# Kernel tuning notes

Measured on AMD Instinct MI355X. Metric: run time of the kernel, lower is better.

The kernel has to match this reference:

```python
import jax, jax.numpy as jnp
import numpy as np

N_EMBD = 1024
HEAD_SIZE = 64
N_HEADS = 16
BLOCK_SIZE = 2048


def setup_inputs() -> dict:
    key = jax.random.key(0)
    ks = jax.random.split(key, 7)
    s = 0.02
    return {
        "X": jax.random.normal(ks[0], (2, BLOCK_SIZE, N_EMBD), dtype=jnp.float32),
        # per-head projection weights, torch Linear layout [out, in] stacked over heads
        "Wq": jax.random.normal(ks[1], (N_HEADS, HEAD_SIZE, N_EMBD), dtype=jnp.float32) * s,
        "Wk": jax.random.normal(ks[2], (N_HEADS, HEAD_SIZE, N_EMBD), dtype=jnp.float32) * s,
        "Wv": jax.random.normal(ks[3], (N_HEADS, HEAD_SIZE, N_EMBD), dtype=jnp.float32) * s,
        "Wp": jax.random.normal(ks[4], (N_EMBD, N_EMBD), dtype=jnp.float32) * s,
        "bp": jax.random.normal(ks[5], (N_EMBD,), dtype=jnp.float32) * s,
    }


def reference(X, Wq, Wk, Wv, Wp, bp):
    B, T, C = X.shape
    # per-head projections: [B,H,T,D]
    q = jnp.einsum("btc,hdc->bhtd", X, Wq)
    k = jnp.einsum("btc,hdc->bhtd", X, Wk)
    v = jnp.einsum("btc,hdc->bhtd", X, Wv)
    # NOTE: original scales by C**-0.5 where C = n_embd (not head_size)
    scores = jnp.einsum("bhtd,bhsd->bhts", q, k) * (C ** -0.5)  # [B,H,T,T]
    causal = jnp.tril(jnp.ones((T, T), dtype=bool))
    scores = jnp.where(causal, scores, -jnp.inf)
    weights = jax.nn.softmax(scores, axis=-1)
    out = jnp.einsum("bhts,bhsd->bhtd", weights, v)  # [B,H,T,D]
    # concat heads along last dim: [B,T,H*D]
    out = out.transpose(0, 2, 1, 3).reshape(B, T, -1)
    # output projection (dropout is identity in eval)
    return out @ Wp.T + bp
```

## Files before the change

### kernel.cpp

```cpp
#include <hip/hip_runtime.h>
#include <hip/hip_bf16.h>

typedef __bf16 bf16_t;
typedef __bf16 bf16x8 __attribute__((ext_vector_type(8)));
typedef __bf16 bf16x4 __attribute__((ext_vector_type(4)));
typedef float  f32x4  __attribute__((ext_vector_type(4)));

#define MFMA16(a,b,c) __builtin_amdgcn_mfma_f32_16x16x32_bf16(a,b,c,0,0,0)

constexpr int B_ = 2, T_ = 2048, H_ = 16, D_ = 64, C_ = 1024;
constexpr int GK = C_;

typedef const __attribute__((address_space(1))) unsigned char ga_t;
typedef __attribute__((address_space(3))) unsigned char la_t;
__device__ __forceinline__ void gld16(const void* g, void* l) {
  __builtin_amdgcn_global_load_lds((ga_t*)g, (la_t*)l, 16, 0, 0);
}

__global__ __launch_bounds__(256) void cast_all(
    const float* __restrict__ X,  const float* __restrict__ Wq,
    const float* __restrict__ Wk, const float* __restrict__ Wv,
    const float* __restrict__ Wp,
    bf16_t* __restrict__ Xb,  bf16_t* __restrict__ Wqb, bf16_t* __restrict__ Wkb,
    bf16_t* __restrict__ Wvb, bf16_t* __restrict__ Wpb)
{
  int i = blockIdx.x * 256 + threadIdx.x;
  const float* src; bf16_t* dst; int off;
  if      (i < 1048576) { src = X;  dst = Xb;  off = i; }
  else if (i < 1310720) { src = Wq; dst = Wqb; off = i - 1048576; }
  else if (i < 1572864) { src = Wk; dst = Wkb; off = i - 1310720; }
  else if (i < 1835008) { src = Wv; dst = Wvb; off = i - 1572864; }
  else                  { src = Wp; dst = Wpb; off = i - 1835008; }
  float4 v = *reinterpret_cast<const float4*>(src + (size_t)off * 4);
  bf16x4 o;
  o[0] = (bf16_t)v.x; o[1] = (bf16_t)v.y; o[2] = (bf16_t)v.z; o[3] = (bf16_t)v.w;
  *reinterpret_cast<bf16x4*>(dst + (size_t)off * 4) = o;
}

__device__ __forceinline__ void gemm_bk64_core(
    const bf16_t* __restrict__ A, const bf16_t* __restrict__ Bw,
    bf16_t* sA, bf16_t* sB, f32x4 (&acc)[4][2], int bm, int bn)
{
  const int tid  = threadIdx.x;
  const int lane = tid & 63, wid = tid >> 6;
  const int wm = wid >> 2, wn = wid & 3;
  const int g = lane >> 4, c = lane & 15;
  const int srow = tid >> 3, scc = tid & 7;
  const int rk = c & 7;

  #define STG(buf, k0)                                                        \
    { char* da = (char*)sA + (buf) * 16384;                                   \
      char* db = (char*)sB + (buf) * 16384;                                   \
      _Pragma("unroll")                                                       \
      for (int it = 0; it < 2; ++it) {                                        \
        int row = it * 64 + srow;                                             \
        int sg  = scc ^ (row & 7);                   \
        int idx = it * 512 + tid;                                             \
        gld16(A  + (size_t)(bm * 128 + row) * GK + (k0) + sg * 8, da + idx * 16); \
        gld16(Bw + (size_t)(bn * 128 + row) * GK + (k0) + sg * 8, db + idx * 16); \
      } }

  STG(0, 0);
  for (int step = 0; step < 16; ++step) {
    const int cur = step & 1;
    __syncthreads();
    if (step < 15) STG(cur ^ 1, (step + 1) * 64);

    const char* ca = (char*)sA + cur * 16384;
    const char* cb = (char*)sB + cur * 16384;
    bf16x8 af[4][2], bf[2][2];
    #pragma unroll
    for (int m = 0; m < 4; ++m) {
      int r = wm * 64 + m * 16 + c;
      #pragma unroll
      for (int ks = 0; ks < 2; ++ks)
        af[m][ks] = *reinterpret_cast<const bf16x8*>(
            ca + r * 128 + (((ks * 4 + g) ^ rk) * 16));
    }
    #pragma unroll
    for (int n = 0; n < 2; ++n) {
      int r = wn * 32 + n * 16 + c;
      #pragma unroll
      for (int ks = 0; ks < 2; ++ks)
        bf[n][ks] = *reinterpret_cast<const bf16x8*>(
            cb + r * 128 + (((ks * 4 + g) ^ rk) * 16));
    }
    __builtin_amdgcn_s_setprio(1);
    #pragma unroll
    for (int ks = 0; ks < 2; ++ks)
      #pragma unroll
      for (int m = 0; m < 4; ++m)
        #pragma unroll
        for (int n = 0; n < 2; ++n)
          acc[m][n] = MFMA16(af[m][ks], bf[n][ks], acc[m][n]);
    __builtin_amdgcn_s_setprio(0);
  }
  #undef STG
}

__global__ __launch_bounds__(512, 4) void gemm_qkv(
    const bf16_t* __restrict__ Xb,
    const bf16_t* __restrict__ Wqb, const bf16_t* __restrict__ Wkb,
    const bf16_t* __restrict__ Wvb,
    bf16_t* __restrict__ qo, bf16_t* __restrict__ ko, bf16_t* __restrict__ vto)
{
  __shared__ bf16_t sA[2][128 * 64];
  __shared__ bf16_t sB[2][128 * 64];
  f32x4 acc[4][2] = {};
  const int mode = blockIdx.z;
  const bf16_t* W = (mode == 0) ? Wqb : (mode == 1) ? Wkb : Wvb;
  gemm_bk64_core(Xb, W, &sA[0][0], &sB[0][0], acc, blockIdx.x, blockIdx.y);

  const int tid = threadIdx.x;
  const int lane = tid & 63, wid = tid >> 6;
  const int wm = wid >> 2, wn = wid & 3;
  const int g = lane >> 4, c = lane & 15;
  const float scale = (mode == 0) ? 0.04508422002778f : 1.0f;
  #pragma unroll
  for (int m = 0; m < 4; ++m) {
    #pragma unroll
    for (int n = 0; n < 2; ++n) {
      #pragma unroll
      for (int r = 0; r < 4; ++r) {
        int row = blockIdx.x * 128 + wm * 64 + m * 16 + g * 4 + r;
        int col = blockIdx.y * 128 + wn * 32 + n * 16 + c;
        int b = row >> 11, t = row & 2047;
        int h = col >> 6,  d = col & 63;
        bf16_t val = (bf16_t)(acc[m][n][r] * scale);
        if (mode == 2)
          vto[((size_t)(b * H_ + h) * D_ + d) * T_ + t] = val;
        else if (mode == 1)
          ko[((size_t)(b * H_ + h) * T_ + t) * D_ + d] = val;
        else
          qo[((size_t)(b * H_ + h) * T_ + t) * D_ + d] = val;
      }
    }
  }
}

__global__ __launch_bounds__(256, 4) void attn_fwd(
    const bf16_t* __restrict__ q, const bf16_t* __restrict__ k,
    const bf16_t* __restrict__ vt, bf16_t* __restrict__ att)
{
  __shared__ bf16_t sK[2][64 * 64], sV[2][64 * 64];
  __shared__ bf16_t sP[4][16 * 64];
  const int tid = threadIdx.x, lane = tid & 63, w = tid >> 6;
  const int g = lane >> 4, c = lane & 15;
  const int bid = blockIdx.x;
  const int qt = 31 - (bid >> 5);
  const int bh = bid & 31;
  const bf16_t* qb = q  + (size_t)bh * T_ * D_;
  const bf16_t* kb = k  + (size_t)bh * T_ * D_;
  const bf16_t* vb = vt + (size_t)bh * D_ * T_;

  bf16x8 qa[2];
  #pragma unroll
  for (int ks = 0; ks < 2; ++ks)
    qa[ks] = *reinterpret_cast<const bf16x8*>(
        qb + (size_t)(qt * 64 + w * 16 + c) * D_ + ks * 32 + g * 8);

  const int srow = tid >> 3, sgr0 = tid & 7;
  #define STAGE(buf, kt)                                                        \
    {                                                                           \
      char* kdst = (char*)sK + (size_t)(buf) * 8192;                            \
      char* vdst = (char*)sV + (size_t)(buf) * 8192;                            \
      _Pragma("unroll")                                                         \
      for (int it = 0; it < 2; ++it) {                                          \
        int idx = it * 256 + tid;                                               \
        int row = it * 32 + srow;                                               \
        int sg  = sgr0 ^ (row & 7);                                             \
        gld16(kb + (size_t)((kt) * 64 + row) * D_ + sg * 8, kdst + idx * 16);   \
        gld16(vb + (size_t)row * T_ + (kt) * 64 + sg * 8,   vdst + idx * 16);   \
      }                                                                         \
    }

  STAGE(0, 0);

  float m_r = -3.0e38f, l_r = 0.f;
  f32x4 acc_t[4] = {};
  const int rowK = c & 7;

  for (int kt = 0; kt <= qt; ++kt) {
    const int cur = kt & 1;
    __syncthreads();
    if (kt < qt) STAGE(cur ^ 1, kt + 1);

    const char* kc = (char*)sK + (size_t)cur * 8192;
    const char* vc = (char*)sV + (size_t)cur * 8192;
    bf16x8 kf[2][4], vf[2][4];
    #pragma unroll
    for (int ks = 0; ks < 2; ++ks)
      #pragma unroll
      for (int f = 0; f < 4; ++f) {
        int rb = (f * 16 + c) * 128;
        int gsw = ((ks * 4 + g) ^ rowK) * 16;
        kf[ks][f] = *reinterpret_cast<const bf16x8*>(kc + rb + gsw);
        vf[ks][f] = *reinterpret_cast<const bf16x8*>(vc + rb + gsw);
      }

    f32x4 s[4] = {};
    #pragma unroll
    for (int fj = 0; fj < 4; ++fj)
      #pragma unroll
      for (int ks = 0; ks < 2; ++ks)
        s[fj] = MFMA16(kf[ks][fj], qa[ks], s[fj]);

    if (kt == qt) {
      #pragma unroll
      for (int fj = 0; fj < 4; ++fj)
        #pragma unroll
        for (int r = 0; r < 4; ++r)
          if (fj * 16 + g * 4 + r > w * 16 + c) s[fj][r] = -1e30f;
    }

    float m01 = fmaxf(fmaxf(s[0][0], s[0][1]), fmaxf(s[0][2], s[0][3]));
    float m23 = fmaxf(fmaxf(s[1][0], s[1][1]), fmaxf(s[1][2], s[1][3]));
    float m45 = fmaxf(fmaxf(s[2][0], s[2][1]), fmaxf(s[2][2], s[2][3]));
    float m67 = fmaxf(fmaxf(s[3][0], s[3][1]), fmaxf(s[3][2], s[3][3]));
    float mx = fmaxf(fmaxf(m01, m23), fmaxf(m45, m67));
    mx = fmaxf(mx, __shfl_xor(mx, 16));
    mx = fmaxf(mx, __shfl_xor(mx, 32));

    if (__any(mx > m_r + 8.f)) {
      float mnew = fmaxf(m_r, mx);
      float sc = __builtin_amdgcn_exp2f(m_r - mnew);
      l_r *= sc;
      #pragma unroll
      for (int fd = 0; fd < 4; ++fd)
        #pragma unroll
        for (int r = 0; r < 4; ++r) acc_t[fd][r] *= sc;
      m_r = mnew;
    }

    char* pc = (char*)sP + (size_t)w * 2048;
    #pragma unroll
    for (int fj = 0; fj < 4; ++fj) {
      bf16x4 pw;
      #pragma unroll
      for (int r = 0; r < 4; ++r) {
        float pe = __builtin_amdgcn_exp2f(s[fj][r] - m_r);
        l_r += pe;
        pw[r] = (bf16_t)pe;
      }
      *reinterpret_cast<bf16x4*>(
          pc + c * 128 + (((fj * 2 + (g >> 1)) ^ rowK) * 16) + (g & 1) * 8) = pw;
    }

    bf16x8 pf[2];
    #pragma unroll
    for (int ks = 0; ks < 2; ++ks)
      pf[ks] = *reinterpret_cast<const bf16x8*>(
          pc + c * 128 + (((ks * 4 + g) ^ rowK) * 16));

    #pragma unroll
    for (int fd = 0; fd < 4; ++fd)
      #pragma unroll
      for (int ks = 0; ks < 2; ++ks)
        acc_t[fd] = MFMA16(vf[ks][fd], pf[ks], acc_t[fd]);
  }

  l_r += __shfl_xor(l_r, 16);
  l_r += __shfl_xor(l_r, 32);
  float inv = 1.0f / l_r;
  const int b = bh >> 4, h = bh & 15;
  const int t = qt * 64 + w * 16 + c;
  #pragma unroll
  for (int fd = 0; fd < 4; ++fd) {
    bf16x4 wv;
    #pragma unroll
    for (int r = 0; r < 4; ++r) wv[r] = (bf16_t)(acc_t[fd][r] * inv);
    int d = fd * 16 + g * 4;
    *reinterpret_cast<bf16x4*>(&att[((size_t)(b * T_ + t) * H_ + h) * D_ + d]) = wv;
  }
  #undef STAGE
}

__global__ __launch_bounds__(512, 4) void gemm_proj(
    const bf16_t* __restrict__ attb, const bf16_t* __restrict__ Wpb,
    const float* __restrict__ bp, float* __restrict__ out)
{
  __shared__ bf16_t sA[2][128 * 64];
  __shared__ bf16_t sB[2][128 * 64];
  f32x4 acc[4][2] = {};
  gemm_bk64_core(attb, Wpb, &sA[0][0], &sB[0][0], acc, blockIdx.x, blockIdx.y);

  const int tid = threadIdx.x;
  const int lane = tid & 63, wid = tid >> 6;
  const int wm = wid >> 2, wn = wid & 3;
  const int g = lane >> 4, c = lane & 15;
  #pragma unroll
  for (int m = 0; m < 4; ++m)
    #pragma unroll
    for (int n = 0; n < 2; ++n)
      #pragma unroll
      for (int r = 0; r < 4; ++r) {
        int row = blockIdx.x * 128 + wm * 64 + m * 16 + g * 4 + r;
        int col = blockIdx.y * 128 + wn * 32 + n * 16 + c;
        out[(size_t)row * C_ + col] = acc[m][n][r] + bp[col];
      }
}

extern "C" void kernel_launch(void* const* d_in, const int* in_sizes, int n_in,
                              void* d_out, int out_size, void* d_ws, size_t ws_size,
                              hipStream_t stream)
{
  const float* X  = (const float*)d_in[0];
  const float* Wq = (const float*)d_in[1];
  const float* Wk = (const float*)d_in[2];
  const float* Wv = (const float*)d_in[3];
  const float* Wp = (const float*)d_in[4];
  const float* bp = (const float*)d_in[5];
  float* out = (float*)d_out;

  char* ws = (char*)d_ws;
  bf16_t* Xb   = (bf16_t*)(ws);
  bf16_t* Wqb  = (bf16_t*)(ws + ((size_t)8  << 20));
  bf16_t* Wkb  = (bf16_t*)(ws + ((size_t)10 << 20));
  bf16_t* Wvb  = (bf16_t*)(ws + ((size_t)12 << 20));
  bf16_t* Wpb  = (bf16_t*)(ws + ((size_t)14 << 20));
  bf16_t* qo   = (bf16_t*)(ws + ((size_t)16 << 20));
  bf16_t* ko   = (bf16_t*)(ws + ((size_t)24 << 20));
  bf16_t* vto  = (bf16_t*)(ws + ((size_t)32 << 20));
  bf16_t* attb = (bf16_t*)(ws + ((size_t)40 << 20));

  cast_all<<<8192, 256, 0, stream>>>(X, Wq, Wk, Wv, Wp, Xb, Wqb, Wkb, Wvb, Wpb);
  gemm_qkv<<<dim3(32, 8, 3), 512, 0, stream>>>(Xb, Wqb, Wkb, Wvb, qo, ko, vto);
  attn_fwd<<<1024, 256, 0, stream>>>(qo, ko, vto, attb);
  gemm_proj<<<dim3(32, 8), 512, 0, stream>>>(attb, Wpb, bp, out);
}
```

Baseline: 105.7 us.

## Fuse QKV projections into one 256x192-tile GEMM with explicit vmcnt pipelining

Replaces the three-way 128x128 QKV GEMM grid with a single kernel. It reads the contiguous Wq/Wk/Wv bf16 buffers as one 3072-row weight and computes 256x192 tiles, so the grid is 256 blocks instead of 768. The main loop uses a hand-scheduled double buffer with s_waitcnt vmcnt, raw barriers and sched_barriers to overlap the global-to-LDS loads with MFMA work. The transposed V output is now written as 4-wide vector stores. The larger tiles raise operand reuse per LDS load but need about 112KB of LDS, which limits occupancy to one block per CU, and the kernel relies on the weight buffers being adjacent in the workspace.

Result: faster. 97.61 us (-7.6%).

```diff
diff --git a/kernel.cpp b/kernel.cpp
--- a/kernel.cpp
+++ b/kernel.cpp
@@ -48,7 +48,7 @@
   const int srow = tid >> 3, scc = tid & 7;
   const int rk = c & 7;
 
-  #define STG(buf, k0)                                                        \
+  #define STG128(buf, k0)                                                     \
     { char* da = (char*)sA + (buf) * 16384;                                   \
       char* db = (char*)sB + (buf) * 16384;                                   \
       _Pragma("unroll")                                                       \
@@ -60,11 +60,11 @@
         gld16(Bw + (size_t)(bn * 128 + row) * GK + (k0) + sg * 8, db + idx * 16); \
       } }
 
-  STG(0, 0);
+  STG128(0, 0);
   for (int step = 0; step < 16; ++step) {
     const int cur = step & 1;
     __syncthreads();
-    if (step < 15) STG(cur ^ 1, (step + 1) * 64);
+    if (step < 15) STG128(cur ^ 1, (step + 1) * 64);
 
     const char* ca = (char*)sA + cur * 16384;
     const char* cb = (char*)sB + cur * 16384;
@@ -95,44 +95,107 @@
           acc[m][n] = MFMA16(af[m][ks], bf[n][ks], acc[m][n]);
     __builtin_amdgcn_s_setprio(0);
   }
+  #undef STG128
+}
+
+__global__ __launch_bounds__(512, 2) void gemm_qkv256(
+    const bf16_t* __restrict__ Xb, const bf16_t* __restrict__ Wqkv,
+    bf16_t* __restrict__ qo, bf16_t* __restrict__ ko, bf16_t* __restrict__ vto)
+{
+  __shared__ bf16_t sA[2][256 * 64];
+  __shared__ bf16_t sB[2][192 * 64];
+  const int tid = threadIdx.x, lane = tid & 63, wid = tid >> 6;
+  const int wm = wid >> 1, wn = wid & 1;
+  const int g = lane >> 4, c = lane & 15, rk = c & 7;
+  const int bx = blockIdx.x, by = blockIdx.y;
+  const int srow = tid >> 3;
+  const int sg   = (tid & 7) ^ (srow & 7);
+  const bf16_t* asrc = Xb   + (size_t)(bx * 256 + srow) * GK + sg * 8;
+  const bf16_t* bsrc = Wqkv + (size_t)(by * 192 + srow) * GK + sg * 8;
+  f32x4 acc[4][6] = {};
+
+  #define STG(buf, kt)                                                        \
+    { char* da = (char*)sA + (buf) * 32768;                                   \
+      char* db = (char*)sB + (buf) * 24576;                                   \
+      _Pragma("unroll")                                                       \
+      for (int it = 0; it < 4; ++it)                                          \
+        gld16(asrc + (size_t)it * 65536 + (kt) * 64, da + (it * 512 + tid) * 16); \
+      _Pragma("unroll")                                                       \
+      for (int it = 0; it < 3; ++it)                                          \
+        gld16(bsrc + (size_t)it * 65536 + (kt) * 64, db + (it * 512 + tid) * 16); \
+    }
+
+  #define ITER(t, buf)                                                        \
+    {                                                                         \
+      if ((t) < 15) asm volatile("s_waitcnt vmcnt(7)");                       \
+      else          asm volatile("s_waitcnt vmcnt(0)");                       \
+      __builtin_amdgcn_s_barrier();             \
+      __builtin_amdgcn_sched_barrier(0);                                      \
+      const char* ca = (const char*)sA + (buf) * 32768;                       \
+      const char* cb = (const char*)sB + (buf) * 24576;                       \
+      bf16x8 af[4][2], bfr[6][2];                                             \
+      _Pragma("unroll")                                                       \
+      for (int mi = 0; mi < 4; ++mi)                                          \
+        _Pragma("unroll")                                                     \
+        for (int ks = 0; ks < 2; ++ks)                                        \
+          af[mi][ks] = *reinterpret_cast<const bf16x8*>(                      \
+              ca + (wm * 64 + mi * 16 + c) * 128 + (((ks * 4 + g) ^ rk) * 16)); \
+      _Pragma("unroll")                                                       \
+      for (int ni = 0; ni < 6; ++ni)                                          \
+        _Pragma("unroll")                                                     \
+        for (int ks = 0; ks < 2; ++ks)                                        \
+          bfr[ni][ks] = *reinterpret_cast<const bf16x8*>(                     \
+              cb + (wn * 96 + ni * 16 + c) * 128 + (((ks * 4 + g) ^ rk) * 16)); \
+      asm volatile("s_waitcnt lgkmcnt(0)");         \
+      __builtin_amdgcn_sched_barrier(0);                                      \
+      __builtin_amdgcn_s_barrier();                \
+      __builtin_amdgcn_sched_barrier(0);                                      \
+      if ((t) + 2 < 16) STG(buf, (t) + 2);           \
+      __builtin_amdgcn_s_setprio(1);                                          \
+      _Pragma("unroll")                                                       \
+      for (int ks = 0; ks < 2; ++ks)                                          \
+        _Pragma("unroll")                                                     \
+        for (int mi = 0; mi < 4; ++mi)                                        \
+          _Pragma("unroll")                                                   \
+          for (int ni = 0; ni < 6; ++ni)                                      \
+            acc[mi][ni] = MFMA16(af[mi][ks], bfr[ni][ks], acc[mi][ni]);       \
+      __builtin_amdgcn_s_setprio(0);                                          \
+    }
+
+  STG(0, 0);
+  STG(1, 1);
+  #pragma unroll 1
+  for (int t0 = 0; t0 < 16; t0 += 2) {
+    ITER(t0, 0);
+    ITER(t0 + 1, 1);
+  }
+  #undef ITER
   #undef STG
-}
-
-__global__ __launch_bounds__(512, 4) void gemm_qkv(
-    const bf16_t* __restrict__ Xb,
-    const bf16_t* __restrict__ Wqb, const bf16_t* __restrict__ Wkb,
-    const bf16_t* __restrict__ Wvb,
-    bf16_t* __restrict__ qo, bf16_t* __restrict__ ko, bf16_t* __restrict__ vto)
-{
-  __shared__ bf16_t sA[2][128 * 64];
-  __shared__ bf16_t sB[2][128 * 64];
-  f32x4 acc[4][2] = {};
-  const int mode = blockIdx.z;
-  const bf16_t* W = (mode == 0) ? Wqb : (mode == 1) ? Wkb : Wvb;
-  gemm_bk64_core(Xb, W, &sA[0][0], &sB[0][0], acc, blockIdx.x, blockIdx.y);
-
-  const int tid = threadIdx.x;
-  const int lane = tid & 63, wid = tid >> 6;
-  const int wm = wid >> 2, wn = wid & 3;
-  const int g = lane >> 4, c = lane & 15;
-  const float scale = (mode == 0) ? 0.04508422002778f : 1.0f;
+
+  const float qscale = 0.04508422002778f;
   #pragma unroll
-  for (int m = 0; m < 4; ++m) {
-    #pragma unroll
-    for (int n = 0; n < 2; ++n) {
-      #pragma unroll
-      for (int r = 0; r < 4; ++r) {
-        int row = blockIdx.x * 128 + wm * 64 + m * 16 + g * 4 + r;
-        int col = blockIdx.y * 128 + wn * 32 + n * 16 + c;
-        int b = row >> 11, t = row & 2047;
-        int h = col >> 6,  d = col & 63;
-        bf16_t val = (bf16_t)(acc[m][n][r] * scale);
-        if (mode == 2)
-          vto[((size_t)(b * H_ + h) * D_ + d) * T_ + t] = val;
-        else if (mode == 1)
-          ko[((size_t)(b * H_ + h) * T_ + t) * D_ + d] = val;
-        else
-          qo[((size_t)(b * H_ + h) * T_ + t) * D_ + d] = val;
+  for (int ni = 0; ni < 6; ++ni) {
+    int col  = by * 192 + wn * 96 + ni * 16 + c;
+    int mode = col >> 10;
+    int cm   = col & 1023;
+    int h = cm >> 6, d = cm & 63;
+    #pragma unroll
+    for (int mi = 0; mi < 4; ++mi) {
+      int row0 = bx * 256 + wm * 64 + mi * 16 + g * 4;
+      int b = row0 >> 11, tt0 = row0 & 2047;
+      if (mode == 2) {
+        bf16x4 wv;
+        #pragma unroll
+        for (int r = 0; r < 4; ++r) wv[r] = (bf16_t)acc[mi][ni][r];
+        *reinterpret_cast<bf16x4*>(
+            &vto[((size_t)(b * H_ + h) * D_ + d) * T_ + tt0]) = wv;
+      } else {
+        bf16_t* dst = (mode == 0) ? qo : ko;
+        float   sc  = (mode == 0) ? qscale : 1.0f;
+        #pragma unroll
+        for (int r = 0; r < 4; ++r)
+          dst[((size_t)(b * H_ + h) * T_ + (tt0 + r)) * D_ + d] =
+              (bf16_t)(acc[mi][ni][r] * sc);
       }
     }
   }
@@ -324,7 +387,7 @@
   bf16_t* attb = (bf16_t*)(ws + ((size_t)40 << 20));
 
   cast_all<<<8192, 256, 0, stream>>>(X, Wq, Wk, Wv, Wp, Xb, Wqb, Wkb, Wvb, Wpb);
-  gemm_qkv<<<dim3(32, 8, 3), 512, 0, stream>>>(Xb, Wqb, Wkb, Wvb, qo, ko, vto);
+  gemm_qkv256<<<dim3(16, 16), 512, 0, stream>>>(Xb, Wqb, qo, ko, vto);
   attn_fwd<<<1024, 256, 0, stream>>>(qo, ko, vto, attb);
   gemm_proj<<<dim3(32, 8), 512, 0, stream>>>(attb, Wpb, bp, out);
 }
```
